# Kernel optimization log

Hardware: AMD Instinct MI355X
Metric: run time of the kernel (lower is better)

Reference implementation:

```python
import jax, jax.numpy as jnp
import numpy as np

B, N, S, D, H = 4, 64, 512, 128, 8  # batch, groups, set size, in_size, heads


def setup_inputs() -> dict:
    key = jax.random.key(0)
    ks = jax.random.split(key, 8)
    s1 = 1.0 / np.sqrt(D)
    s2 = 1.0 / np.sqrt(2 * D)
    return {
        "x": jax.random.normal(ks[0], (B, N, S, D), jnp.float32),
        # DeepSets phi MLP: D -> D -> D -> D (hidden=[in_size,in_size])
        "w1": jax.random.normal(ks[1], (D, D), jnp.float32) * s1,
        "b1": jnp.zeros((D,), jnp.float32),
        "w2": jax.random.normal(ks[2], (D, D), jnp.float32) * s1,
        "b2": jnp.zeros((D,), jnp.float32),
        "w3": jax.random.normal(ks[3], (D, D), jnp.float32) * s1,
        "b3": jnp.zeros((D,), jnp.float32),
        # attention projection: 2D -> H*D
        "W": jax.random.normal(ks[4], (2 * D, H * D), jnp.float32) * s2,
        "Wb": jnp.zeros((H * D,), jnp.float32),
        # per-head query vector (zeros-init in original; random for a nontrivial baseline)
        "q": jax.random.normal(ks[5], (H, D), jnp.float32) * 0.1,
    }


def reference(x, w1, b1, w2, b2, w3, b3, W, Wb, q):
    # SetTransform (DeepSets): per-element MLP then sum over set dim (-2)
    h = jax.nn.relu(x @ w1 + b1)
    h = jax.nn.relu(h @ w2 + b2)
    h = h @ w3 + b3
    set_feat = h.sum(axis=-2)                                  # (B, N, D)
    sf = jnp.broadcast_to(set_feat[..., None, :], x.shape)      # (B, N, S, D)
    comb = jnp.concatenate([x, sf], axis=-1)                    # (B, N, S, 2D)
    heads = (comb @ W + Wb).reshape(B, N, S, H, D)              # (B, N, S, H, D)
    e = jnp.einsum('bnshd,hd->bnsh', heads, q)                  # (B, N, S, H)
    return jax.nn.softmax(e, axis=-2)                           # softmax over set dim
```

## Files before the change

kernel.cpp:

```cpp
#include <hip/hip_runtime.h>

#define Bsz 4
#define Ngrp 64
#define Sset 512
#define Din 128
#define Hh 8
#define EST (Sset + 1)

typedef float f32x4 __attribute__((ext_vector_type(4)));

#define DPP_QUAD_XOR1 0xB1
#define DPP_QUAD_XOR2 0x4E
#define DPP_ROW_HALF_MIRROR 0x141
#define DPP_ROW_MIRROR 0x140

template <int CTRL>
__device__ __forceinline__ float dpp_add(float v) {
    int perm = __builtin_amdgcn_update_dpp(0, __float_as_int(v), CTRL, 0xF, 0xF, true);
    return v + __int_as_float(perm);
}

__device__ __forceinline__ float row16_sum(float v) {
    v = dpp_add<DPP_QUAD_XOR1>(v);
    v = dpp_add<DPP_QUAD_XOR2>(v);
    v = dpp_add<DPP_ROW_HALF_MIRROR>(v);
    v = dpp_add<DPP_ROW_MIRROR>(v);
    return v;
}

__global__ void __launch_bounds__(256) compute_u_kernel(
    const float* __restrict__ W,
    const float* __restrict__ q,
    float* __restrict__ u)
{
    const int tid = threadIdx.x;
    const int grp = tid >> 4;
    const int sub = tid & 15;

    const int idx = blockIdx.x * 16 + grp;
    const int h = idx >> 7;
    const int c = idx & 127;

    const float4* Wr = (const float4*)(W + (size_t)c * (Hh * Din) + (size_t)h * Din);
    const float4* qr = (const float4*)(q + h * Din);
    const float4 w0 = Wr[sub];
    const float4 w1 = Wr[sub + 16];
    const float4 q0 = qr[sub];
    const float4 q1 = qr[sub + 16];

    float v;
    v = w0.x * q0.x;
    v = fmaf(w0.y, q0.y, v);
    v = fmaf(w0.z, q0.z, v);
    v = fmaf(w0.w, q0.w, v);
    v = fmaf(w1.x, q1.x, v);
    v = fmaf(w1.y, q1.y, v);
    v = fmaf(w1.z, q1.z, v);
    v = fmaf(w1.w, q1.w, v);
    v = row16_sum(v);
    if (sub == 0) u[idx] = v;
}

__global__ void __launch_bounds__(1024) attn_softmax_kernel(
    const float* __restrict__ x,
    const float* __restrict__ u,
    float* __restrict__ out)
{
    const int bn = blockIdx.x;
    const int tid = threadIdx.x;
    const int wave = tid >> 6;
    const int lane = tid & 63;
    const int g    = lane >> 4;
    const int sub  = lane & 15;

    __shared__ __align__(16) float e_s[Hh * EST];

    const f32x4* xb = (const f32x4*)(x + (size_t)bn * Sset * Din);

    const int rbase = wave * 32 + g;
    f32x4 px0[4], px1[4];
#pragma unroll
    for (int i = 0; i < 4; ++i) {
        const f32x4* xr = xb + (size_t)(rbase + i * 4) * 32;
        px0[i] = __builtin_nontemporal_load(xr + sub);
        px1[i] = __builtin_nontemporal_load(xr + sub + 16);
    }

    const float4* u4 = (const float4*)u;
    float4 ua[Hh], ub[Hh];
#pragma unroll
    for (int h = 0; h < Hh; ++h) {
        ua[h] = u4[h * 32 + sub];
        ub[h] = u4[h * 32 + sub + 16];
    }

#pragma unroll
    for (int pass = 0; pass < 8; ++pass) {
        const f32x4 x0 = px0[pass & 3];
        const f32x4 x1 = px1[pass & 3];
        if (pass < 4) {
            const f32x4* xr = xb + (size_t)(rbase + (pass + 4) * 4) * 32;
            px0[pass & 3] = __builtin_nontemporal_load(xr + sub);
            px1[pass & 3] = __builtin_nontemporal_load(xr + sub + 16);
        }
        const int r = rbase + pass * 4;

        float st = 0.f;
#pragma unroll
        for (int h = 0; h < Hh; ++h) {
            float v;
            v = x0.x * ua[h].x;
            v = fmaf(x0.y, ua[h].y, v);
            v = fmaf(x0.z, ua[h].z, v);
            v = fmaf(x0.w, ua[h].w, v);
            v = fmaf(x1.x, ub[h].x, v);
            v = fmaf(x1.y, ub[h].y, v);
            v = fmaf(x1.z, ub[h].z, v);
            v = fmaf(x1.w, ub[h].w, v);
            v = row16_sum(v);
            if (sub == h) st = v;
        }
        if (sub < Hh) e_s[sub * EST + r] = st;
    }
    __syncthreads();

    if (wave < Hh) {
        float* eh = &e_s[wave * EST];

        float m = -1e30f;
#pragma unroll
        for (int k = 0; k < Sset / 64; ++k) m = fmaxf(m, eh[lane + 64 * k]);
#pragma unroll
        for (int off = 32; off >= 1; off >>= 1) m = fmaxf(m, __shfl_xor(m, off, 64));

        float p[Sset / 64];
        float sum = 0.f;
#pragma unroll
        for (int k = 0; k < Sset / 64; ++k) {
            p[k] = __expf(eh[lane + 64 * k] - m);
            sum += p[k];
        }
#pragma unroll
        for (int off = 32; off >= 1; off >>= 1) sum += __shfl_xor(sum, off, 64);

        const float inv = 1.f / sum;
#pragma unroll
        for (int k = 0; k < Sset / 64; ++k) eh[lane + 64 * k] = p[k] * inv;
    }
    __syncthreads();

    {
        const int s = tid >> 1;
        const int half = tid & 1;
        float4 o;
        o.x = e_s[(half * 4 + 0) * EST + s];
        o.y = e_s[(half * 4 + 1) * EST + s];
        o.z = e_s[(half * 4 + 2) * EST + s];
        o.w = e_s[(half * 4 + 3) * EST + s];
        ((float4*)(out + ((size_t)bn * Sset + s) * Hh))[half] = o;
    }
}

extern "C" void kernel_launch(void* const* d_in, const int* in_sizes, int n_in,
                              void* d_out, int out_size, void* d_ws, size_t ws_size,
                              hipStream_t stream) {
    const float* x = (const float*)d_in[0];
    const float* W = (const float*)d_in[7];
    const float* q = (const float*)d_in[9];
    float* u = (float*)d_ws;
    float* out = (float*)d_out;

    compute_u_kernel<<<dim3(64), dim3(256), 0, stream>>>(W, q, u);
    attn_softmax_kernel<<<dim3(Bsz * Ngrp), dim3(1024), 0, stream>>>(x, u, out);
}
```

Measured before the change: 117.8 us.

## Fuse u = W·q precompute into attention-softmax kernel via shared memory

New measurement: 118.4 us. Within noise of the previous version (+0.4%).

```diff
diff --git a/kernel.cpp b/kernel.cpp
--- a/kernel.cpp
+++ b/kernel.cpp
@@ -6,8 +6,6 @@
 #define Din 128
 #define Hh 8
 #define EST (Sset + 1)
-
-typedef float f32x4 __attribute__((ext_vector_type(4)));
 
 #define DPP_QUAD_XOR1 0xB1
 #define DPP_QUAD_XOR2 0x4E
@@ -28,42 +26,10 @@
     return v;
 }
 
-__global__ void __launch_bounds__(256) compute_u_kernel(
+__global__ void __launch_bounds__(1024) fused_attn_kernel(
+    const float* __restrict__ x,
     const float* __restrict__ W,
     const float* __restrict__ q,
-    float* __restrict__ u)
-{
-    const int tid = threadIdx.x;
-    const int grp = tid >> 4;
-    const int sub = tid & 15;
-
-    const int idx = blockIdx.x * 16 + grp;
-    const int h = idx >> 7;
-    const int c = idx & 127;
-
-    const float4* Wr = (const float4*)(W + (size_t)c * (Hh * Din) + (size_t)h * Din);
-    const float4* qr = (const float4*)(q + h * Din);
-    const float4 w0 = Wr[sub];
-    const float4 w1 = Wr[sub + 16];
-    const float4 q0 = qr[sub];
-    const float4 q1 = qr[sub + 16];
-
-    float v;
-    v = w0.x * q0.x;
-    v = fmaf(w0.y, q0.y, v);
-    v = fmaf(w0.z, q0.z, v);
-    v = fmaf(w0.w, q0.w, v);
-    v = fmaf(w1.x, q1.x, v);
-    v = fmaf(w1.y, q1.y, v);
-    v = fmaf(w1.z, q1.z, v);
-    v = fmaf(w1.w, q1.w, v);
-    v = row16_sum(v);
-    if (sub == 0) u[idx] = v;
-}
-
-__global__ void __launch_bounds__(1024) attn_softmax_kernel(
-    const float* __restrict__ x,
-    const float* __restrict__ u,
     float* __restrict__ out)
 {
     const int bn = blockIdx.x;
@@ -72,21 +38,49 @@
     const int lane = tid & 63;
     const int g    = lane >> 4;
     const int sub  = lane & 15;
+    const int grp  = tid >> 4;
 
+    __shared__ __align__(16) float u_s[Hh * Din];
     __shared__ __align__(16) float e_s[Hh * EST];
 
-    const f32x4* xb = (const f32x4*)(x + (size_t)bn * Sset * Din);
+    {
+        const float4* q4 = (const float4*)q;
+        float4 w0, w1, nw0, nw1;
+        {
+            const float4* Wr = (const float4*)(W + (size_t)grp * (Hh * Din));
+            w0 = Wr[sub];
+            w1 = Wr[sub + 16];
+        }
+#pragma unroll
+        for (int p = 0; p < 16; ++p) {
+            if (p < 15) {
+                const int cn = (((p + 1) & 1) << 6) + grp;
+                const int hn = (p + 1) >> 1;
+                const float4* Wrn = (const float4*)(W + (size_t)cn * (Hh * Din) + (size_t)hn * Din);
+                nw0 = Wrn[sub];
+                nw1 = Wrn[sub + 16];
+            }
+            const int h = p >> 1;
+            const float4 q0 = q4[h * 32 + sub];
+            const float4 q1 = q4[h * 32 + sub + 16];
+            float v;
+            v = w0.x * q0.x;
+            v = fmaf(w0.y, q0.y, v);
+            v = fmaf(w0.z, q0.z, v);
+            v = fmaf(w0.w, q0.w, v);
+            v = fmaf(w1.x, q1.x, v);
+            v = fmaf(w1.y, q1.y, v);
+            v = fmaf(w1.z, q1.z, v);
+            v = fmaf(w1.w, q1.w, v);
+            v = row16_sum(v);
+            if (sub == 0) u_s[p * 64 + grp] = v;
+            w0 = nw0;
+            w1 = nw1;
+        }
+    }
+    __syncthreads();
 
-    const int rbase = wave * 32 + g;
-    f32x4 px0[4], px1[4];
-#pragma unroll
-    for (int i = 0; i < 4; ++i) {
-        const f32x4* xr = xb + (size_t)(rbase + i * 4) * 32;
-        px0[i] = __builtin_nontemporal_load(xr + sub);
-        px1[i] = __builtin_nontemporal_load(xr + sub + 16);
-    }
-
-    const float4* u4 = (const float4*)u;
+    const float4* u4 = (const float4*)u_s;
     float4 ua[Hh], ub[Hh];
 #pragma unroll
     for (int h = 0; h < Hh; ++h) {
@@ -94,14 +88,24 @@
         ub[h] = u4[h * 32 + sub + 16];
     }
 
+    const float4* xb = (const float4*)(x + (size_t)bn * Sset * Din);
+    const int rbase = wave * 32 + g;
+    float4 px0[4], px1[4];
+#pragma unroll
+    for (int i = 0; i < 4; ++i) {
+        const float4* xr = xb + (size_t)(rbase + i * 4) * 32;
+        px0[i] = xr[sub];
+        px1[i] = xr[sub + 16];
+    }
+
 #pragma unroll
     for (int pass = 0; pass < 8; ++pass) {
-        const f32x4 x0 = px0[pass & 3];
-        const f32x4 x1 = px1[pass & 3];
+        const float4 x0 = px0[pass & 3];
+        const float4 x1 = px1[pass & 3];
         if (pass < 4) {
-            const f32x4* xr = xb + (size_t)(rbase + (pass + 4) * 4) * 32;
-            px0[pass & 3] = __builtin_nontemporal_load(xr + sub);
-            px1[pass & 3] = __builtin_nontemporal_load(xr + sub + 16);
+            const float4* xr = xb + (size_t)(rbase + (pass + 4) * 4) * 32;
+            px0[pass & 3] = xr[sub];
+            px1[pass & 3] = xr[sub + 16];
         }
         const int r = rbase + pass * 4;
 
@@ -167,9 +171,7 @@
     const float* x = (const float*)d_in[0];
     const float* W = (const float*)d_in[7];
     const float* q = (const float*)d_in[9];
-    float* u = (float*)d_ws;
     float* out = (float*)d_out;
 
-    compute_u_kernel<<<dim3(64), dim3(256), 0, stream>>>(W, q, u);
-    attn_softmax_kernel<<<dim3(Bsz * Ngrp), dim3(1024), 0, stream>>>(x, u, out);
+    fused_attn_kernel<<<dim3(Bsz * Ngrp), dim3(1024), 0, stream>>>(x, W, q, out);
 }
```
